# Performance work log

Measured on AMD Instinct MI355X. Metric: run time of the kernel, lower is better.

Reference implementation:

```python
import jax, jax.numpy as jnp
import numpy as np

B, S, H, I, E = 2, 2048, 1024, 4096, 8


def setup_inputs() -> dict:
    key = jax.random.key(0)
    k1, k2, k3, k4 = jax.random.split(key, 4)
    hidden_states = jax.random.normal(k1, (B, S, H), dtype=jnp.float32)
    # router: nn.Linear(H, E, bias=False) -> weight (E, H)
    Wr = jax.random.normal(k2, (E, H), dtype=jnp.float32) * 0.02
    # per-expert MLP: Linear(H,I) weight (I,H); Linear(I,H) weight (H,I); stacked over E
    W1 = jax.random.normal(k3, (E, I, H), dtype=jnp.float32) * 0.02
    W2 = jax.random.normal(k4, (E, H, I), dtype=jnp.float32) * 0.02
    return {"hidden_states": hidden_states, "Wr": Wr, "W1": W1, "W2": W2}


def reference(hidden_states, Wr, W1, W2):
    b, s, h = hidden_states.shape
    n_exp = Wr.shape[0]
    x = hidden_states.reshape(-1, h)                      # (N, H)
    logits = x @ Wr.T                                     # (N, E)
    probs = jax.nn.softmax(logits, axis=-1)               # (N, E)
    # top_k with k == num_experts: sorted probs descending (one-hot mask then
    # covers every expert, so each expert sees every token; expert i's output is
    # weighted by the i-th largest prob, exactly as the torch code does).
    top_probs, _ = jax.lax.top_k(probs, n_exp)            # (N, E)
    hmid = jnp.einsum('nh,eih->nei', x, W1)               # (N, E, I)
    hmid = jax.nn.gelu(hmid, approximate=False)           # exact erf GELU (torch nn.GELU default)
    yexp = jnp.einsum('nei,ehi->neh', hmid, W2)           # (N, E, H)
    out = jnp.einsum('neh,ne->nh', yexp, top_probs)       # weighted combine
    return out.reshape(b, s, h)
```

## Files before the change

### kernel.cpp

```cpp
#include <hip/hip_runtime.h>
#include <hip/hip_bf16.h>

#define NTOK 4096
#define HD   1024
#define ID   4096
#define NE   8
#define LDH  (NE * ID)

typedef float  floatx4 __attribute__((ext_vector_type(4)));
typedef __bf16 bf16x8  __attribute__((ext_vector_type(8)));
typedef unsigned short u16;

__device__ __forceinline__ u16 f2bf(float f) {
    union { float f; unsigned int i; } c; c.f = f;
    return (u16)((c.i + 0x7fffu + ((c.i >> 16) & 1u)) >> 16);
}

__device__ __forceinline__ void async_copy16(u16* lds, const u16* g) {
    __builtin_amdgcn_global_load_lds(
        (const __attribute__((address_space(1))) void*)g,
        (__attribute__((address_space(3))) void*)lds, 16, 0, 0);
}

__device__ __forceinline__ float gelu_fast(float v) {
    const float u = v * (0.7978845608f + 0.0356774081f * v * v);
    const float t = 1.f - 2.f / (__expf(2.f * u) + 1.f);
    return 0.5f * v * (1.f + t);
}

__global__ __launch_bounds__(256) void convert_kernel(
    const float* __restrict__ src, u16* __restrict__ dst)
{
    const size_t i = ((size_t)blockIdx.x * 256 + threadIdx.x) * 8;
    const float4 a = *(const float4*)(src + i);
    const float4 b = *(const float4*)(src + i + 4);
    ushort4 o0, o1;
    o0.x = f2bf(a.x); o0.y = f2bf(a.y); o0.z = f2bf(a.z); o0.w = f2bf(a.w);
    o1.x = f2bf(b.x); o1.y = f2bf(b.y); o1.z = f2bf(b.z); o1.w = f2bf(b.w);
    *(ushort4*)(dst + i)     = o0;
    *(ushort4*)(dst + i + 4) = o1;
}

__global__ __launch_bounds__(256) void router_kernel(
    const float* __restrict__ x, const float* __restrict__ Wr,
    float* __restrict__ wbuf)
{
    const int n    = blockIdx.x * 4 + (threadIdx.x >> 6);
    const int lane = threadIdx.x & 63;
    const float* xr = x + (size_t)n * HD;
    float acc[NE];
#pragma unroll
    for (int e = 0; e < NE; ++e) acc[e] = 0.f;
    for (int h = lane; h < HD; h += 64) {
        const float xv = xr[h];
#pragma unroll
        for (int e = 0; e < NE; ++e) acc[e] += xv * Wr[e * HD + h];
    }
#pragma unroll
    for (int e = 0; e < NE; ++e) {
        float v = acc[e];
#pragma unroll
        for (int off = 32; off > 0; off >>= 1) v += __shfl_xor(v, off, 64);
        acc[e] = v;
    }
    float mx = acc[0];
#pragma unroll
    for (int e = 1; e < NE; ++e) mx = fmaxf(mx, acc[e]);
    float s = 0.f;
#pragma unroll
    for (int e = 0; e < NE; ++e) { acc[e] = __expf(acc[e] - mx); s += acc[e]; }
    const float inv = 1.f / s;
#pragma unroll
    for (int e = 0; e < NE; ++e) acc[e] *= inv;
#pragma unroll
    for (int i = 0; i < NE - 1; ++i)
#pragma unroll
        for (int j = 0; j < NE - 1 - i; ++j) {
            const float a = acc[j], b = acc[j + 1];
            acc[j] = fmaxf(a, b); acc[j + 1] = fminf(a, b);
        }
    if (lane < NE) wbuf[lane * NTOK + n] = acc[lane];
}

__device__ __forceinline__ void gemm_tile(
    const u16* __restrict__ A, const u16* __restrict__ B,
    int ldA, int ldB, int kb, int ke, int rowBase, int colBase,
    u16* As, u16* Bs, floatx4 acc[4][4])
{
    const int t    = threadIdx.x;
    const int w    = t >> 6;
    const int lane = t & 63;
    const int wm   = w & 1, wn = w >> 1;
    const int quad = lane >> 4, l15 = lane & 15;
    const int srow = lane >> 2;
    const int scol = (lane & 3) << 3;

    const u16* gA = A + (size_t)(rowBase + w * 16 + srow) * ldA + kb + scol;
    const u16* gB = B + (size_t)(colBase + w * 16 + srow) * ldB + kb + scol;
    u16* ldsA = As + w * 512;
    u16* ldsB = Bs + w * 512;
    const size_t rstepA = (size_t)64 * ldA;
    const size_t rstepB = (size_t)64 * ldB;

    int aoff[4], boff[4];
#pragma unroll
    for (int i = 0; i < 4; ++i) {
        aoff[i] = (wm * 64 + i * 16 + l15) * 32 + quad * 8;
        boff[i] = (wn * 64 + i * 16 + l15) * 32 + quad * 8;
    }

    for (int k0 = kb; k0 < ke; k0 += 32) {
        async_copy16(ldsA,         gA);
        async_copy16(ldsA + 2048,  gA + rstepA);
        async_copy16(ldsB,         gB);
        async_copy16(ldsB + 2048,  gB + rstepB);
        gA += 32; gB += 32;
        __syncthreads();
        bf16x8 af[4], bfr[4];
#pragma unroll
        for (int i = 0; i < 4; ++i) {
            af[i]  = *(const bf16x8*)(As + aoff[i]);
            bfr[i] = *(const bf16x8*)(Bs + boff[i]);
        }
#pragma unroll
        for (int mi = 0; mi < 4; ++mi)
#pragma unroll
            for (int ni = 0; ni < 4; ++ni)
                acc[mi][ni] = __builtin_amdgcn_mfma_f32_16x16x32_bf16(
                    af[mi], bfr[ni], acc[mi][ni], 0, 0, 0);
        __syncthreads();
    }
}

__global__ __launch_bounds__(256) void gemm1_kernel(
    const u16* __restrict__ X, const u16* __restrict__ W1b,
    const float* __restrict__ wbuf, u16* __restrict__ hmid)
{
    __shared__ __align__(16) u16 As[128 * 32];
    __shared__ __align__(16) u16 Bs[128 * 32];
    floatx4 acc[4][4] = {};
    const int rowBase = blockIdx.y * 128, colBase = blockIdx.x * 128;
    const int e = colBase >> 12;
    gemm_tile(X, W1b, HD, HD, 0, HD, rowBase, colBase, As, Bs, acc);

    const int t = threadIdx.x, w = t >> 6, lane = t & 63;
    const int wm = w & 1, wn = w >> 1, quad = lane >> 4, l15 = lane & 15;
#pragma unroll
    for (int mi = 0; mi < 4; ++mi)
#pragma unroll
        for (int r = 0; r < 4; ++r) {
            const int row = rowBase + wm * 64 + mi * 16 + quad * 4 + r;
            const float wv = wbuf[e * NTOK + row];
#pragma unroll
            for (int ni = 0; ni < 4; ++ni) {
                const int col = colBase + wn * 64 + ni * 16 + l15;
                const float v = gelu_fast(acc[mi][ni][r]);
                hmid[(size_t)row * LDH + col] = f2bf(v * wv);
            }
        }
}

__global__ __launch_bounds__(256) void gemm2_kernel(
    const u16* __restrict__ hmid, const u16* __restrict__ W2b,
    float* __restrict__ accbuf)
{
    __shared__ __align__(16) u16 As[128 * 32];
    __shared__ __align__(16) u16 Bs[128 * 32];
    floatx4 acc[4][4] = {};
    const int rowBase = blockIdx.x * 128;
    const int colBase = blockIdx.y * 128;
    const int z = blockIdx.z;
    for (int ee = 0; ee < 2; ++ee) {
        const int e = 2 * z + ee;
        gemm_tile(hmid + (size_t)e * ID, W2b + (size_t)e * HD * ID,
                  LDH, ID, 0, ID, rowBase, colBase, As, Bs, acc);
    }

    float* accs = accbuf + (size_t)z * NTOK * HD;
    const int t = threadIdx.x, w = t >> 6, lane = t & 63;
    const int wm = w & 1, wn = w >> 1, quad = lane >> 4, l15 = lane & 15;
#pragma unroll
    for (int mi = 0; mi < 4; ++mi)
#pragma unroll
        for (int r = 0; r < 4; ++r) {
            const int row = rowBase + wm * 64 + mi * 16 + quad * 4 + r;
#pragma unroll
            for (int ni = 0; ni < 4; ++ni) {
                const int col = colBase + wn * 64 + ni * 16 + l15;
                accs[(size_t)row * HD + col] = acc[mi][ni][r];
            }
        }
}

__global__ __launch_bounds__(256) void finalize_kernel(
    const float* __restrict__ accbuf, float* __restrict__ out)
{
    const size_t NH = (size_t)NTOK * HD;
    const size_t i = ((size_t)blockIdx.x * 256 + threadIdx.x) * 4;
    const float4 a = *(const float4*)(accbuf + i);
    const float4 b = *(const float4*)(accbuf + NH + i);
    const float4 c = *(const float4*)(accbuf + 2 * NH + i);
    const float4 d = *(const float4*)(accbuf + 3 * NH + i);
    float4 o;
    o.x = a.x + b.x + c.x + d.x; o.y = a.y + b.y + c.y + d.y;
    o.z = a.z + b.z + c.z + d.z; o.w = a.w + b.w + c.w + d.w;
    *(float4*)(out + i) = o;
}

extern "C" void kernel_launch(void* const* d_in, const int* in_sizes, int n_in,
                              void* d_out, int out_size, void* d_ws, size_t ws_size,
                              hipStream_t stream) {
    const float* x  = (const float*)d_in[0];
    const float* Wr = (const float*)d_in[1];
    const float* W1 = (const float*)d_in[2];
    const float* W2 = (const float*)d_in[3];
    float* out = (float*)d_out;

    const size_t MB = 1024 * 1024;
    char* ws = (char*)d_ws;
    float* wbuf   = (float*)ws;
    u16*   Xb     = (u16*)(ws + 131072);
    u16*   W1b    = (u16*)(ws + 131072 + 8 * MB);
    u16*   W2b    = (u16*)(ws + 131072 + 72 * MB);
    u16*   hmid   = (u16*)(ws + 131072 + 136 * MB);
    float* accbuf = (float*)(ws + 131072 + 392 * MB);
    if (ws_size < 131072 + 456 * MB) return;

    convert_kernel<<<dim3((NTOK * HD) / 2048), 256, 0, stream>>>(x, Xb);
    convert_kernel<<<dim3((NE * ID * HD) / 2048), 256, 0, stream>>>(W1, W1b);
    convert_kernel<<<dim3((NE * HD * ID) / 2048), 256, 0, stream>>>(W2, W2b);
    router_kernel<<<dim3(NTOK / 4), 256, 0, stream>>>(x, Wr, wbuf);

    gemm1_kernel<<<dim3(NE * ID / 128, NTOK / 128), 256, 0, stream>>>(
        Xb, W1b, wbuf, hmid);
    gemm2_kernel<<<dim3(NTOK / 128, HD / 128, 4), 256, 0, stream>>>(
        hmid, W2b, accbuf);
    finalize_kernel<<<dim3(NTOK * HD / 1024), 256, 0, stream>>>(accbuf, out);
}
```

Baseline: 1.169 ms.

## Use 256x256 double-buffered MFMA tiles with swizzled LDS and block remapping

Replaces the 128x128 single-buffered GEMM tile with a 256x256 tile run by 512 threads. Global-to-LDS async copies are double-buffered and overlapped with MFMA work through explicit vmcnt waits and raw barriers. The LDS layout is XOR-swizzled to avoid bank conflicts, priority hints are set around the MFMA blocks, and a grouped block-index remap improves L2 reuse. The larger tiles cut global traffic per FLOP, but they raise register pressure (32 accumulators per thread) and rely on fragile hand-written waitcnt synchronisation.

```diff
diff --git a/kernel.cpp b/kernel.cpp
--- a/kernel.cpp
+++ b/kernel.cpp
@@ -27,6 +27,12 @@
     const float t = 1.f - 2.f / (__expf(2.f * u) + 1.f);
     return 0.5f * v * (1.f + t);
 }
+
+#define FENCE()  asm volatile("" ::: "memory")
+#define BAR()    do { FENCE(); __builtin_amdgcn_s_barrier(); FENCE(); } while (0)
+#define WAITV4() asm volatile("s_waitcnt vmcnt(4)" ::: "memory")
+#define WAITV0() asm volatile("s_waitcnt vmcnt(0)" ::: "memory")
+#define WAITL0() asm volatile("s_waitcnt lgkmcnt(0)" ::: "memory")
 
 __global__ __launch_bounds__(256) void convert_kernel(
     const float* __restrict__ src, u16* __restrict__ dst)
@@ -82,108 +88,162 @@
     if (lane < NE) wbuf[lane * NTOK + n] = acc[lane];
 }
 
-__device__ __forceinline__ void gemm_tile(
+__device__ __forceinline__ void gemm256_tile(
     const u16* __restrict__ A, const u16* __restrict__ B,
-    int ldA, int ldB, int kb, int ke, int rowBase, int colBase,
-    u16* As, u16* Bs, floatx4 acc[4][4])
+    int ldA, int ldB, int K, int rowBase, int colBase,
+    u16* As0, u16* As1, u16* Bs0, u16* Bs1,
+    floatx4 acc[8][4])
 {
     const int t    = threadIdx.x;
-    const int w    = t >> 6;
-    const int lane = t & 63;
+    const int w    = t >> 6, lane = t & 63;
     const int wm   = w & 1, wn = w >> 1;
     const int quad = lane >> 4, l15 = lane & 15;
-    const int srow = lane >> 2;
-    const int scol = (lane & 3) << 3;
-
-    const u16* gA = A + (size_t)(rowBase + w * 16 + srow) * ldA + kb + scol;
-    const u16* gB = B + (size_t)(colBase + w * 16 + srow) * ldB + kb + scol;
-    u16* ldsA = As + w * 512;
-    u16* ldsB = Bs + w * 512;
-    const size_t rstepA = (size_t)64 * ldA;
-    const size_t rstepB = (size_t)64 * ldB;
-
-    int aoff[4], boff[4];
-#pragma unroll
-    for (int i = 0; i < 4; ++i) {
-        aoff[i] = (wm * 64 + i * 16 + l15) * 32 + quad * 8;
-        boff[i] = (wn * 64 + i * 16 + l15) * 32 + quad * 8;
-    }
-
-    for (int k0 = kb; k0 < ke; k0 += 32) {
-        async_copy16(ldsA,         gA);
-        async_copy16(ldsA + 2048,  gA + rstepA);
-        async_copy16(ldsB,         gB);
-        async_copy16(ldsB + 2048,  gB + rstepB);
-        gA += 32; gB += 32;
-        __syncthreads();
-        bf16x8 af[4], bfr[4];
-#pragma unroll
-        for (int i = 0; i < 4; ++i) {
-            af[i]  = *(const bf16x8*)(As + aoff[i]);
-            bfr[i] = *(const bf16x8*)(Bs + boff[i]);
-        }
+
+    const int srow   = (w << 4) + (lane >> 2);
+    const int schunk = ((lane & 3) ^ ((lane >> 3) & 3)) << 3;
+    const u16* gA = A + (size_t)(rowBase + srow) * ldA + schunk;
+    const u16* gB = B + (size_t)(colBase + srow) * ldB + schunk;
+    const size_t hA = (size_t)128 * ldA, hB = (size_t)128 * ldB;
+    u16* lA0 = As0 + w * 512;
+    u16* lA1 = As1 + w * 512;
+    u16* lB0 = Bs0 + w * 512;
+    u16* lB1 = Bs1 + w * 512;
+
+    const int sw = (l15 >> 1) & 3;
+    int aoff[8], boff[4];
+#pragma unroll
+    for (int mi = 0; mi < 8; ++mi)
+        aoff[mi] = (wm * 128 + mi * 16 + l15) * 32 + ((quad ^ sw) << 3);
+#pragma unroll
+    for (int ni = 0; ni < 4; ++ni)
+        boff[ni] = (wn * 64 + ni * 16 + l15) * 32 + ((quad ^ sw) << 3);
+
+#define STAGE2(lA, lB, kt) do { const int _ko = (kt) << 5;          \
+        async_copy16(lA,        gA + _ko);                          \
+        async_copy16(lA + 4096, gA + _ko + hA);                     \
+        async_copy16(lB,        gB + _ko);                          \
+        async_copy16(lB + 4096, gB + _ko + hB); } while (0)
+
+    const int nkt = K >> 5;
+    bf16x8 af[8], bfr[4];
+    STAGE2(lA0, lB0, 0);
+    STAGE2(lA1, lB1, 1);
+
+#pragma unroll 1
+    for (int kt = 0; kt < nkt; kt += 2) {
+        WAITV4(); BAR();
+#pragma unroll
+        for (int mi = 0; mi < 8; ++mi) af[mi] = *(const bf16x8*)(As0 + aoff[mi]);
+#pragma unroll
+        for (int ni = 0; ni < 4; ++ni) bfr[ni] = *(const bf16x8*)(Bs0 + boff[ni]);
+        WAITL0();
+        __builtin_amdgcn_s_setprio(1);
 #pragma unroll
         for (int mi = 0; mi < 4; ++mi)
 #pragma unroll
             for (int ni = 0; ni < 4; ++ni)
                 acc[mi][ni] = __builtin_amdgcn_mfma_f32_16x16x32_bf16(
                     af[mi], bfr[ni], acc[mi][ni], 0, 0, 0);
-        __syncthreads();
-    }
-}
-
-__global__ __launch_bounds__(256) void gemm1_kernel(
+        __builtin_amdgcn_s_setprio(0);
+        BAR();
+        if (kt + 2 < nkt) STAGE2(lA0, lB0, kt + 2);
+        __builtin_amdgcn_s_setprio(1);
+#pragma unroll
+        for (int mi = 4; mi < 8; ++mi)
+#pragma unroll
+            for (int ni = 0; ni < 4; ++ni)
+                acc[mi][ni] = __builtin_amdgcn_mfma_f32_16x16x32_bf16(
+                    af[mi], bfr[ni], acc[mi][ni], 0, 0, 0);
+        __builtin_amdgcn_s_setprio(0);
+        if (kt + 2 < nkt) { WAITV4(); } else { WAITV0(); }
+        BAR();
+#pragma unroll
+        for (int mi = 0; mi < 8; ++mi) af[mi] = *(const bf16x8*)(As1 + aoff[mi]);
+#pragma unroll
+        for (int ni = 0; ni < 4; ++ni) bfr[ni] = *(const bf16x8*)(Bs1 + boff[ni]);
+        WAITL0();
+        __builtin_amdgcn_s_setprio(1);
+#pragma unroll
+        for (int mi = 0; mi < 4; ++mi)
+#pragma unroll
+            for (int ni = 0; ni < 4; ++ni)
+                acc[mi][ni] = __builtin_amdgcn_mfma_f32_16x16x32_bf16(
+                    af[mi], bfr[ni], acc[mi][ni], 0, 0, 0);
+        __builtin_amdgcn_s_setprio(0);
+        BAR();
+        if (kt + 3 < nkt) STAGE2(lA1, lB1, kt + 3);
+        __builtin_amdgcn_s_setprio(1);
+#pragma unroll
+        for (int mi = 4; mi < 8; ++mi)
+#pragma unroll
+            for (int ni = 0; ni < 4; ++ni)
+                acc[mi][ni] = __builtin_amdgcn_mfma_f32_16x16x32_bf16(
+                    af[mi], bfr[ni], acc[mi][ni], 0, 0, 0);
+        __builtin_amdgcn_s_setprio(0);
+    }
+#undef STAGE2
+}
+
+__global__ __launch_bounds__(512, 2) void gemm1_kernel(
     const u16* __restrict__ X, const u16* __restrict__ W1b,
     const float* __restrict__ wbuf, u16* __restrict__ hmid)
 {
-    __shared__ __align__(16) u16 As[128 * 32];
-    __shared__ __align__(16) u16 Bs[128 * 32];
-    floatx4 acc[4][4] = {};
-    const int rowBase = blockIdx.y * 128, colBase = blockIdx.x * 128;
+    __shared__ __align__(16) u16 As[2][8192];
+    __shared__ __align__(16) u16 Bs[2][8192];
+    floatx4 acc[8][4] = {};
+    const int bid = blockIdx.x;
+    const int swz = (bid & 7) * 256 + (bid >> 3);
+    const int mt = swz >> 7, nt = swz & 127;
+    const int rowBase = mt * 256, colBase = nt * 256;
     const int e = colBase >> 12;
-    gemm_tile(X, W1b, HD, HD, 0, HD, rowBase, colBase, As, Bs, acc);
+
+    gemm256_tile(X, W1b, HD, HD, HD, rowBase, colBase,
+                 As[0], As[1], Bs[0], Bs[1], acc);
 
     const int t = threadIdx.x, w = t >> 6, lane = t & 63;
     const int wm = w & 1, wn = w >> 1, quad = lane >> 4, l15 = lane & 15;
 #pragma unroll
-    for (int mi = 0; mi < 4; ++mi)
+    for (int mi = 0; mi < 8; ++mi)
 #pragma unroll
         for (int r = 0; r < 4; ++r) {
-            const int row = rowBase + wm * 64 + mi * 16 + quad * 4 + r;
+            const int row = rowBase + wm * 128 + mi * 16 + quad * 4 + r;
             const float wv = wbuf[e * NTOK + row];
 #pragma unroll
             for (int ni = 0; ni < 4; ++ni) {
                 const int col = colBase + wn * 64 + ni * 16 + l15;
-                const float v = gelu_fast(acc[mi][ni][r]);
-                hmid[(size_t)row * LDH + col] = f2bf(v * wv);
+                hmid[(size_t)row * LDH + col] =
+                    f2bf(gelu_fast(acc[mi][ni][r]) * wv);
             }
         }
 }
 
-__global__ __launch_bounds__(256) void gemm2_kernel(
+__global__ __launch_bounds__(512, 2) void gemm2_kernel(
     const u16* __restrict__ hmid, const u16* __restrict__ W2b,
     float* __restrict__ accbuf)
 {
-    __shared__ __align__(16) u16 As[128 * 32];
-    __shared__ __align__(16) u16 Bs[128 * 32];
-    floatx4 acc[4][4] = {};
-    const int rowBase = blockIdx.x * 128;
-    const int colBase = blockIdx.y * 128;
-    const int z = blockIdx.z;
+    __shared__ __align__(16) u16 As[2][8192];
+    __shared__ __align__(16) u16 Bs[2][8192];
+    floatx4 acc[8][4] = {};
+    const int bid = blockIdx.x;
+    const int swz = (bid & 7) * 32 + (bid >> 3);
+    const int z = swz >> 6, mt = (swz >> 2) & 15, nt = swz & 3;
+    const int rowBase = mt * 256, colBase = nt * 256;
+
     for (int ee = 0; ee < 2; ++ee) {
         const int e = 2 * z + ee;
-        gemm_tile(hmid + (size_t)e * ID, W2b + (size_t)e * HD * ID,
-                  LDH, ID, 0, ID, rowBase, colBase, As, Bs, acc);
+        gemm256_tile(hmid + (size_t)e * ID, W2b + (size_t)e * HD * ID,
+                     LDH, ID, ID, rowBase, colBase,
+                     As[0], As[1], Bs[0], Bs[1], acc);
     }
 
     float* accs = accbuf + (size_t)z * NTOK * HD;
     const int t = threadIdx.x, w = t >> 6, lane = t & 63;
     const int wm = w & 1, wn = w >> 1, quad = lane >> 4, l15 = lane & 15;
 #pragma unroll
-    for (int mi = 0; mi < 4; ++mi)
+    for (int mi = 0; mi < 8; ++mi)
 #pragma unroll
         for (int r = 0; r < 4; ++r) {
-            const int row = rowBase + wm * 64 + mi * 16 + quad * 4 + r;
+            const int row = rowBase + wm * 128 + mi * 16 + quad * 4 + r;
 #pragma unroll
             for (int ni = 0; ni < 4; ++ni) {
                 const int col = colBase + wn * 64 + ni * 16 + l15;
@@ -231,9 +291,9 @@
     convert_kernel<<<dim3((NE * HD * ID) / 2048), 256, 0, stream>>>(W2, W2b);
     router_kernel<<<dim3(NTOK / 4), 256, 0, stream>>>(x, Wr, wbuf);
 
-    gemm1_kernel<<<dim3(NE * ID / 128, NTOK / 128), 256, 0, stream>>>(
+    gemm1_kernel<<<dim3(NE * ID / 256 * (NTOK / 256)), 512, 0, stream>>>(
         Xb, W1b, wbuf, hmid);
-    gemm2_kernel<<<dim3(NTOK / 128, HD / 128, 4), 256, 0, stream>>>(
+    gemm2_kernel<<<dim3((NTOK / 256) * (HD / 256) * 4), 512, 0, stream>>>(
         hmid, W2b, accbuf);
     finalize_kernel<<<dim3(NTOK * HD / 1024), 256, 0, stream>>>(accbuf, out);
 }
```

Result: faster. 974.1 us (-16.7%).
